# Kernel optimization log

Hardware: AMD Instinct MI355X
Metric: run time of the kernel (lower is better)

The kernel has to match this reference:

```python
import jax, jax.numpy as jnp
import numpy as np

BITS = 4
GROUP = 128
IN = 4096
OUT = 14336
B = 64
PACK = 32 // BITS          # 8 values per int32
MAXQ = (1 << BITS) - 1     # 15


def setup_inputs() -> dict:
    key = jax.random.key(0)
    k = jax.random.split(key, 5)
    x = jax.random.normal(k[0], (B, IN), dtype=jnp.float32)
    # non-negative int32 so arithmetic right-shift behaves like logical shift
    qweight = jax.random.randint(k[1], (IN // PACK, OUT), 0, 2**31 - 1, dtype=jnp.int32)
    qzeros = jax.random.randint(k[2], (IN // GROUP, OUT // PACK), 0, 2**31 - 1, dtype=jnp.int32)
    scales = jax.random.uniform(k[3], (IN // GROUP, OUT), dtype=jnp.float32,
                                minval=1e-3, maxval=1e-2)
    bias = jax.random.normal(k[4], (OUT,), dtype=jnp.float32) * 0.01
    g_idx = (jnp.arange(IN) // GROUP).astype(jnp.int32)
    return dict(x=x, qweight=qweight, qzeros=qzeros, scales=scales, bias=bias, g_idx=g_idx)


def _dequant(qweight, qzeros, scales, g_idx):
    shifts = jnp.arange(PACK, dtype=jnp.int32) * BITS  # [PACK]
    # unpack weights: [IN//PACK, PACK, OUT] -> [IN, OUT]
    w = (qweight[:, None, :] >> shifts[None, :, None]) & MAXQ
    w = w.reshape(IN, OUT)
    # unpack zeros: [G, OUT//PACK, PACK] -> [G, OUT]; pack() stored (zeros-1), so add 1 back
    z = (qzeros[:, :, None] >> shifts[None, None, :]) & MAXQ
    z = z.reshape(-1, OUT) + 1
    # per-group dequant with arbitrary g_idx (act-order support)
    return scales[g_idx] * (w - z[g_idx]).astype(scales.dtype)


def reference(x, qweight, qzeros, scales, bias, g_idx):
    W = _dequant(qweight, qzeros, scales, g_idx)  # [IN, OUT]
    return x @ W + bias
```

## Files before the change

### kernel.cpp

```cpp
#include <hip/hip_runtime.h>
#include <hip/hip_bf16.h>

using u32 = unsigned int;
using u16 = unsigned short;

typedef __attribute__((ext_vector_type(8))) _Float16 half8;
typedef __attribute__((ext_vector_type(2))) _Float16 half2v;
typedef __attribute__((ext_vector_type(16))) float f32x16;
typedef __attribute__((ext_vector_type(4))) u32 u32x4;

#define IN_K   4096
#define OUT_N  14336
#define NST    16

__global__ __launch_bounds__(256) void prep_kernel(const float* __restrict__ x,
                                                   u16* __restrict__ xs) {
  const int t = blockIdx.x * 256 + threadIdx.x;
  const int c = t >> 6;
  const int r = t & 63;
  const float* px = x + r * IN_K + c * 8;
  const float4 a = *(const float4*)px;
  const float4 b = *(const float4*)(px + 4);
  const float af[4] = {a.x, a.y, a.z, a.w};
  const float bf[4] = {b.x, b.y, b.z, b.w};
  union { u32x4 v; u32 u[4]; } o;
#pragma unroll
  for (int i = 0; i < 4; ++i) {
    const _Float16 hl = (_Float16)af[i];
    const _Float16 hh = (_Float16)bf[i];
    u16 lo, hi;
    __builtin_memcpy(&lo, &hl, 2);
    __builtin_memcpy(&hi, &hh, 2);
    o.u[i] = (u32)lo | ((u32)hi << 16);
  }
  *(u32x4*)(xs + (size_t)t * 8) = o.v;
}

static __device__ __forceinline__ half8 dequant8(u32 q, half2v hz, half2v s2) {
  const u32 p0 = (q & 0x000F000Fu) | 0x64006400u;
  const u32 p1 = ((q >> 4) & 0x000F000Fu) | 0x64006400u;
  const u32 p2 = ((q >> 8) & 0x000F000Fu) | 0x64006400u;
  const u32 p3 = ((q >> 12) & 0x000F000Fu) | 0x64006400u;
  half2v t0, t1, t2, t3;
  __builtin_memcpy(&t0, &p0, 4);
  __builtin_memcpy(&t1, &p1, 4);
  __builtin_memcpy(&t2, &p2, 4);
  __builtin_memcpy(&t3, &p3, 4);
  union { half8 v; half2v h[4]; } bb;
  bb.h[0] = (t0 - hz) * s2;
  bb.h[1] = (t1 - hz) * s2;
  bb.h[2] = (t2 - hz) * s2;
  bb.h[3] = (t3 - hz) * s2;
  return bb.v;
}

__global__ __launch_bounds__(512, 4) void qgemm_kernel(
    const u32* __restrict__ qw, const u32* __restrict__ qz,
    const float* __restrict__ scal, const u16* __restrict__ xs,
    const float* __restrict__ bias, float* __restrict__ out) {
  __shared__ alignas(16) char smem[81920];
  const int tid = threadIdx.x;
  const int lane = tid & 63;
  const int g = lane >> 5;
  const int nn = lane & 31;
  const int wv = tid >> 6;
  const int ch = wv & 1;
  const int kq = wv >> 1;
  const int tq = tid & 127;
  const int bx = blockIdx.x;
  const int colabs = bx * 64 + ch * 32 + nn;
  const int zsh = (nn & 7) * 4;
  char* const base = smem + kq * 20480;

  f32x16 acc0, acc1;
#pragma unroll
  for (int i = 0; i < 16; ++i) { acc0[i] = 0.f; acc1[i] = 0.f; }

  float sv[8]; u32 zv[8];
#pragma unroll
  for (int t = 0; t < 8; ++t) {
    sv[t] = scal[(size_t)(kq * 8 + t) * OUT_N + colabs];
    zv[t] = qz[(size_t)(kq * 8 + t) * (OUT_N / 8) + (colabs >> 3)];
  }
  asm volatile("s_waitcnt vmcnt(0)" ::: "memory");

  auto issue = [&](int st) {
    const int slot = st & 1;
    char* ab = base + slot * 8192;
    char* qb = base + 16384 + slot * 2048;
    const u16* asrc = xs + (size_t)(kq * 128 + st * 8) * 512;
#pragma unroll
    for (int r = 0; r < 4; ++r) {
      const int p = r * 128 + tq;
      __builtin_amdgcn_global_load_lds(
          (const __attribute__((address_space(1))) void*)(asrc + p * 8),
          (__attribute__((address_space(3))) void*)(ab + p * 16), 16, 0, 0);
    }
    const int j = tq >> 4, cg = tq & 15;
    const u32* qsrc = qw + (size_t)(kq * 128 + st * 8 + j) * OUT_N
                         + bx * 64 + cg * 4;
    __builtin_amdgcn_global_load_lds(
        (const __attribute__((address_space(1))) void*)qsrc,
        (__attribute__((address_space(3))) void*)(qb + tq * 16), 16, 0, 0);
  };

  issue(0); issue(1);

#pragma unroll
  for (int st = 0; st < NST; ++st) {
    if (st < NST - 1)
      asm volatile("s_waitcnt vmcnt(5)" ::: "memory");
    else
      asm volatile("s_waitcnt vmcnt(0)" ::: "memory");
    __builtin_amdgcn_s_barrier();
    asm volatile("" ::: "memory");

    const int gi = st >> 1;
    const u32 zq = (zv[gi] >> zsh) & 0xFu;
    const u32 hzu = 0x64016401u + zq * 0x00010001u;
    half2v hz; __builtin_memcpy(&hz, &hzu, 4);
    const _Float16 hs = (_Float16)sv[gi];
    const half2v s2 = {hs, hs};

    const u16* ab = (const u16*)(base + (st & 1) * 8192);
    const u32* qb = (const u32*)(base + 16384 + (st & 1) * 2048);
    __builtin_amdgcn_s_setprio(1);
#pragma unroll
    for (int s = 0; s < 4; ++s) {
      const int cl = s * 2 + g;
      const half8 a0 = *(const half8*)(ab + (cl * 64 + nn) * 8);
      const half8 a1 = *(const half8*)(ab + (cl * 64 + nn + 32) * 8);
      const u32 q = qb[cl * 64 + ch * 32 + nn];
      const half8 bb = dequant8(q, hz, s2);
      acc0 = __builtin_amdgcn_mfma_f32_32x32x16_f16(a0, bb, acc0, 0, 0, 0);
      acc1 = __builtin_amdgcn_mfma_f32_32x32x16_f16(a1, bb, acc1, 0, 0, 0);
    }
    __builtin_amdgcn_s_setprio(0);

    if (st + 2 < NST) {
      __builtin_amdgcn_s_barrier();
      asm volatile("" ::: "memory");
      issue(st + 2);
    }
  }

  __syncthreads();
  float* ep = (float*)smem + kq * 4096;
#pragma unroll
  for (int r = 0; r < 16; ++r) {
    const int row0 = (r & 3) + 8 * (r >> 2) + 4 * g;
    ep[row0 * 64 + ch * 32 + nn] = acc0[r];
    ep[(row0 + 32) * 64 + ch * 32 + nn] = acc1[r];
  }
  __syncthreads();
  const int pos = tid * 8;
  const int row = pos >> 6;
  const int colb = pos & 63;
  const float* eb = (const float*)smem;
  float4 v0 = *(const float4*)(bias + bx * 64 + colb);
  float4 v1 = *(const float4*)(bias + bx * 64 + colb + 4);
#pragma unroll
  for (int q = 0; q < 4; ++q) {
    const float4 a = *(const float4*)(eb + q * 4096 + pos);
    const float4 b = *(const float4*)(eb + q * 4096 + pos + 4);
    v0.x += a.x; v0.y += a.y; v0.z += a.z; v0.w += a.w;
    v1.x += b.x; v1.y += b.y; v1.z += b.z; v1.w += b.w;
  }
  float* po = out + (size_t)row * OUT_N + bx * 64 + colb;
  *(float4*)po = v0;
  *(float4*)(po + 4) = v1;
}

extern "C" void kernel_launch(void* const* d_in, const int* in_sizes, int n_in,
                              void* d_out, int out_size, void* d_ws, size_t ws_size,
                              hipStream_t stream) {
  (void)in_sizes; (void)n_in; (void)out_size; (void)ws_size;
  const float* x    = (const float*)d_in[0];
  const u32*   qw   = (const u32*)d_in[1];
  const u32*   qz   = (const u32*)d_in[2];
  const float* sc   = (const float*)d_in[3];
  const float* bias = (const float*)d_in[4];
  float* out = (float*)d_out;
  u16* xs = (u16*)d_ws;

  prep_kernel<<<128, 256, 0, stream>>>(x, xs);
  qgemm_kernel<<<224, 512, 0, stream>>>(qw, qz, sc, xs, bias, out);
}
```

Measured before the change: 26.36 us.

## Stage global loads through registers instead of direct global-to-LDS loads

Replaces the direct global_load_lds double-buffered pipeline with a register-staged prefetch. The next stage is loaded into VGPRs while the current one computes, then written to LDS after a barrier. This drops the vmcnt waits tied to direct-to-LDS loads and allows vectorized LDS stores. The cost is extra registers, which may reduce occupancy under launch_bounds(512,4), plus a second barrier per stage.

```diff
diff --git a/kernel.cpp b/kernel.cpp
--- a/kernel.cpp
+++ b/kernel.cpp
@@ -82,39 +82,35 @@
     sv[t] = scal[(size_t)(kq * 8 + t) * OUT_N + colabs];
     zv[t] = qz[(size_t)(kq * 8 + t) * (OUT_N / 8) + (colabs >> 3)];
   }
-  asm volatile("s_waitcnt vmcnt(0)" ::: "memory");
 
-  auto issue = [&](int st) {
-    const int slot = st & 1;
-    char* ab = base + slot * 8192;
-    char* qb = base + 16384 + slot * 2048;
-    const u16* asrc = xs + (size_t)(kq * 128 + st * 8) * 512;
+  auto loadStage = [&](int st, u32x4* ra, u32x4& rq) {
+    const char* asrc = (const char*)(xs + (size_t)(kq * 128 + st * 8) * 512);
 #pragma unroll
-    for (int r = 0; r < 4; ++r) {
-      const int p = r * 128 + tq;
-      __builtin_amdgcn_global_load_lds(
-          (const __attribute__((address_space(1))) void*)(asrc + p * 8),
-          (__attribute__((address_space(3))) void*)(ab + p * 16), 16, 0, 0);
-    }
+    for (int r = 0; r < 4; ++r)
+      ra[r] = *(const u32x4*)(asrc + (r * 128 + tq) * 16);
     const int j = tq >> 4, cg = tq & 15;
-    const u32* qsrc = qw + (size_t)(kq * 128 + st * 8 + j) * OUT_N
-                         + bx * 64 + cg * 4;
-    __builtin_amdgcn_global_load_lds(
-        (const __attribute__((address_space(1))) void*)qsrc,
-        (__attribute__((address_space(3))) void*)(qb + tq * 16), 16, 0, 0);
+    rq = *(const u32x4*)(qw + (size_t)(kq * 128 + st * 8 + j) * OUT_N
+                            + bx * 64 + cg * 4);
+  };
+  auto writeStage = [&](int st, const u32x4* ra, u32x4 rq) {
+    char* ab = base + (st & 1) * 8192;
+#pragma unroll
+    for (int r = 0; r < 4; ++r)
+      *(u32x4*)(ab + (r * 128 + tq) * 16) = ra[r];
+    char* qb = base + 16384 + (st & 1) * 2048;
+    *(u32x4*)(qb + tq * 16) = rq;
   };
 
-  issue(0); issue(1);
+  u32x4 ra[2][4]; u32x4 rq[2];
+  loadStage(0, ra[0], rq[0]);
+  writeStage(0, ra[0], rq[0]);
+  loadStage(1, ra[1], rq[1]);
+  asm volatile("s_waitcnt lgkmcnt(0)" ::: "memory");
+  __builtin_amdgcn_s_barrier();
+  asm volatile("" ::: "memory");
 
 #pragma unroll
   for (int st = 0; st < NST; ++st) {
-    if (st < NST - 1)
-      asm volatile("s_waitcnt vmcnt(5)" ::: "memory");
-    else
-      asm volatile("s_waitcnt vmcnt(0)" ::: "memory");
-    __builtin_amdgcn_s_barrier();
-    asm volatile("" ::: "memory");
-
     const int gi = st >> 1;
     const u32 zq = (zv[gi] >> zsh) & 0xFu;
     const u32 hzu = 0x64016401u + zq * 0x00010001u;
@@ -137,10 +133,15 @@
     }
     __builtin_amdgcn_s_setprio(0);
 
-    if (st + 2 < NST) {
+    if (st + 1 < NST) {
       __builtin_amdgcn_s_barrier();
       asm volatile("" ::: "memory");
-      issue(st + 2);
+      writeStage(st + 1, ra[(st + 1) & 1], rq[(st + 1) & 1]);
+      if (st + 2 < NST)
+        loadStage(st + 2, ra[st & 1], rq[st & 1]);
+      asm volatile("s_waitcnt lgkmcnt(0)" ::: "memory");
+      __builtin_amdgcn_s_barrier();
+      asm volatile("" ::: "memory");
     }
   }
 
```

Result: no change. 26.88 us (+2.0%).
